# Kernel tuning notes

Hardware: AMD Instinct MI355X
Metric: run time of the kernel (lower is better)

## Reference

```python
import jax, jax.numpy as jnp
import numpy as np

B = 65536
NC = 64          # coarse samples
NF = 128         # fine samples
NEAR, FAR = 2.0, 6.0


def setup_inputs() -> dict:
    key = jax.random.key(0)
    k1, k2, k3, k4, k5, k6 = jax.random.split(key, 6)
    ray_origin = jax.random.normal(k1, (B, 3), dtype=jnp.float32)
    ray_direction = jax.random.normal(k2, (B, 3), dtype=jnp.float32)
    # stratified linspace depths, as in the coarse branch of _sample_points_on_ray
    step = (FAR - NEAR) / (NC - 1)
    coarse_depth_values = jnp.broadcast_to(
        NEAR + jnp.arange(NC, dtype=jnp.float32) * step, (B, NC)
    )
    coarse_weights = jax.random.uniform(k3, (B, NC), dtype=jnp.float32)
    u = jax.random.uniform(k4, (B, NF), dtype=jnp.float32)
    raw_density = jax.random.uniform(k5, (B, NC + NF, 1), dtype=jnp.float32)
    raw_color = jax.random.uniform(k6, (B, NC + NF, 3), dtype=jnp.float32)
    return {
        "ray_origin": ray_origin,
        "ray_direction": ray_direction,
        "coarse_depth_values": coarse_depth_values,
        "coarse_weights": coarse_weights,
        "u": u,
        "raw_density": raw_density,
        "raw_color": raw_color,
    }


def _sample_pdf(bins, weights, u):
    """Inverse-CDF sampling. bins: [B, M+1], weights: [B, M], u: [B, N]."""
    M = weights.shape[1]
    weights = weights + 1e-5
    pdf = weights / jnp.sum(weights, axis=-1, keepdims=True)
    cdf = jnp.cumsum(pdf, axis=-1)                     # [B, M]
    cdf = jnp.concatenate([jnp.zeros_like(cdf[:, :1]), cdf], axis=-1)  # [B, M+1]
    # torch loop `above_inds += (u >= cdf[:, i])` for i in [0, M) ==
    # searchsorted(cdf[:, :M], u, side='right')
    above = jax.vmap(lambda c, uu: jnp.searchsorted(c, uu, side="right"))(
        cdf[:, :M], u
    )                                                  # [B, N], values in [1, M]
    below = jnp.clip(above - 1, 0, None)
    cdf_b = jnp.take_along_axis(cdf, below, axis=-1)
    cdf_a = jnp.take_along_axis(cdf, above, axis=-1)
    bins_b = jnp.take_along_axis(bins, below, axis=-1)
    bins_a = jnp.take_along_axis(bins, above, axis=-1)
    denom = cdf_a - cdf_b
    denom = jnp.where(denom < 1e-5, jnp.ones_like(denom), denom)
    t = (u - cdf_b) / denom
    return bins_b + t * (bins_a - bins_b)


def _composite(raw_density, raw_color, depth_values):
    # distances between consecutive samples, last one = 1e10
    dists = depth_values[..., 1:] - depth_values[..., :-1]
    dists = jnp.concatenate(
        [dists, jnp.full_like(dists[:, :1], 1e10)], axis=-1
    )
    alpha = 1.0 - jnp.exp(-raw_density[..., 0] * dists)          # [B, S]
    T = jnp.cumprod(1.0 - alpha + 1e-10, axis=-1)[:, :-1]
    T = jnp.concatenate([jnp.ones_like(T[:, :1]), T], axis=-1)
    weights = T * alpha                                           # [B, S]
    depth = jnp.sum(weights * depth_values, axis=-1, keepdims=True)
    color = jnp.sum(weights[..., None] * raw_color, axis=-2)      # [B, 3]
    return depth, color, weights


def reference(ray_origin, ray_direction, coarse_depth_values, coarse_weights,
              u, raw_density, raw_color):
    # fine branch of _sample_points_on_ray
    mids = 0.5 * (coarse_depth_values[..., 1:] + coarse_depth_values[..., :-1])
    w = coarse_weights[:, 1:-1]
    fine_depths = _sample_pdf(mids, w, u)                         # [B, NF]
    depth_values = jnp.sort(
        jnp.concatenate([coarse_depth_values, fine_depths], axis=-1), axis=-1
    )                                                             # [B, NC+NF]
    points_on_ray = (
        ray_origin[:, None, :]
        + ray_direction[:, None, :] * depth_values[..., None]
    )                                                             # [B, S, 3]
    depth, color_map, weights = _composite(raw_density, raw_color, depth_values)
    # forward of RenderRay returns the color map; points kept live via dummy use
    del points_on_ray, depth, weights
    return color_map
```

## Files before the change

### kernel.cpp

```cpp
#include <hip/hip_runtime.h>

#define NC 64
#define NF 128
#define NT 192
#define B_TOTAL 65536
#define RPB 4

#define NEAR_F 2.0f
#define STEP_F (4.0f / 63.0f)
#define INV_STEP (63.0f / 4.0f)

__global__ __launch_bounds__(256) void render_ray_kernel(
    const float* __restrict__ cw,
    const float* __restrict__ u_in,
    const float* __restrict__ dens,
    const float* __restrict__ col,
    float* __restrict__ out)
{
    const int wave = threadIdx.x >> 6;
    const int lane = threadIdx.x & 63;
    const int ray  = blockIdx.x * RPB + wave;

    __shared__ float s_cdf [RPB][64];
    __shared__ float s_m   [RPB][200];
    __shared__ int   s_hist[RPB][64];

    const float wraw = cw[(size_t)ray * NC + lane];
    float x = u_in[(size_t)ray * NF + lane];
    float y = u_in[(size_t)ray * NF + 64 + lane];

    const float wv = (lane >= 1 && lane <= 62) ? (wraw + 1e-5f) : 0.0f;
    float ssum = wv;
    #pragma unroll
    for (int off = 32; off; off >>= 1) ssum += __shfl_xor(ssum, off);
    const float pdf = __fdividef(wv, ssum);
    float scan = pdf;
    #pragma unroll
    for (int off = 1; off < 64; off <<= 1) {
        const float t = __shfl_up(scan, off);
        if (lane >= off) scan += t;
    }
    s_cdf[wave][lane]  = scan;
    s_hist[wave][lane] = 0;
    __syncthreads();

    #pragma unroll
    for (int k = 2; k <= 128; k <<= 1) {
        #pragma unroll
        for (int j = k >> 1; j > 0; j >>= 1) {
            if (j == 64) {
                const float mn = fminf(x, y);
                const float mx = fmaxf(x, y);
                x = mn; y = mx;
            } else {
                const bool lower = (lane & j) == 0;
                const bool ascx  = (k >= 128) ? true : ((lane & k) == 0);
                const bool ascy  = (k >= 128) ? true
                                 : ((k == 64) ? false : ((lane & k) == 0));
                const float px = __shfl_xor(x, j);
                const float py = __shfl_xor(y, j);
                x = (ascx == lower) ? fminf(x, px) : fmaxf(x, px);
                y = (ascy == lower) ? fminf(y, py) : fmaxf(y, py);
            }
        }
    }

    const float* __restrict__ cdfp = s_cdf[wave];
    auto sample = [&](float u) -> float {
        int l = 0, h = 62;
        while (l < h) {
            const int mid = (l + h) >> 1;
            if (cdfp[mid] <= u) l = mid + 1; else h = mid;
        }
        const int below = l - 1;
        const float cb = cdfp[below];
        const float ca = cdfp[l];
        float denom = ca - cb;
        if (denom < 1e-5f) denom = 1.0f;
        const float t = __fdividef(u - cb, denom);
        return NEAR_F + ((float)below + 0.5f + t) * STEP_F;
    };

    const float fx = sample(x);
    const float fy = sample(y);
    int gx = (int)floorf((fx - NEAR_F) * INV_STEP) + 1;
    int gy = (int)floorf((fy - NEAR_F) * INV_STEP) + 1;
    gx = min(max(gx, 1), 63);
    gy = min(max(gy, 1), 63);

    s_m[wave][lane + gx]      = fx;
    s_m[wave][lane + 64 + gy] = fy;
    atomicAdd(&s_hist[wave][gx], 1);
    atomicAdd(&s_hist[wave][gy], 1);
    __syncthreads();

    int hsum = s_hist[wave][lane];
    #pragma unroll
    for (int off = 1; off < 64; off <<= 1) {
        const int t = __shfl_up(hsum, off);
        if (lane >= off) hsum += t;
    }
    s_m[wave][lane + hsum] = NEAR_F + (float)lane * STEP_F;
    __syncthreads();

    const float* __restrict__ mp = s_m[wave];
    const int i0 = 3 * lane;
    const float m0 = mp[i0], m1 = mp[i0 + 1], m2 = mp[i0 + 2];
    const float m3 = mp[i0 + 3];
    const float d0 = m1 - m0;
    const float d1 = m2 - m1;
    const float d2 = (lane == 63) ? 1e10f : (m3 - m2);

    const float* __restrict__ dp = dens + (size_t)ray * NT + i0;
    const float a0 = 1.0f - __expf(-dp[0] * d0);
    const float a1 = 1.0f - __expf(-dp[1] * d1);
    const float a2 = 1.0f - __expf(-dp[2] * d2);
    const float f0 = 1.0f - a0 + 1e-10f;
    const float f1 = 1.0f - a1 + 1e-10f;
    const float f2 = 1.0f - a2 + 1e-10f;

    float scanp = f0 * f1 * f2;
    #pragma unroll
    for (int off = 1; off < 64; off <<= 1) {
        const float t = __shfl_up(scanp, off);
        if (lane >= off) scanp *= t;
    }
    float T0 = __shfl_up(scanp, 1);
    if (lane == 0) T0 = 1.0f;
    const float T1 = T0 * f0;
    const float T2 = T1 * f1;

    const float w0 = T0 * (1.0f - f0 + 1e-10f);
    const float w1 = T1 * (1.0f - f1 + 1e-10f);
    const float w2 = T2 * (1.0f - f2 + 1e-10f);

    const float* __restrict__ cp = col + (size_t)ray * NT * 3 + 3 * (size_t)i0;
    float ax = w0 * cp[0] + w1 * cp[3] + w2 * cp[6];
    float ay = w0 * cp[1] + w1 * cp[4] + w2 * cp[7];
    float az = w0 * cp[2] + w1 * cp[5] + w2 * cp[8];

    #pragma unroll
    for (int off = 32; off; off >>= 1) {
        ax += __shfl_xor(ax, off);
        ay += __shfl_xor(ay, off);
        az += __shfl_xor(az, off);
    }
    if (lane == 0) {
        out[(size_t)ray * 3 + 0] = ax;
        out[(size_t)ray * 3 + 1] = ay;
        out[(size_t)ray * 3 + 2] = az;
    }
}

extern "C" void kernel_launch(void* const* d_in, const int* in_sizes, int n_in,
                              void* d_out, int out_size, void* d_ws, size_t ws_size,
                              hipStream_t stream) {
    const float* cwts = (const float*)d_in[3];
    const float* u    = (const float*)d_in[4];
    const float* dens = (const float*)d_in[5];
    const float* col  = (const float*)d_in[6];
    float* out = (float*)d_out;

    dim3 grid(B_TOTAL / RPB);
    dim3 block(256);
    hipLaunchKernelGGL(render_ray_kernel, grid, block, 0, stream,
                       cwts, u, dens, col, out);
}
```

Baseline: 285.9 us.

## Use DPP wave scans, wave-level barriers, and branchless fixed-depth search

Replaces the shuffle-based prefix scans with DPP row_shr/row_bcast scans and swaps the block-wide __syncthreads for wave barriers, since each wave works on its own ray and shared slice. It also makes the binary search a fixed-depth unrolled loop, computes the insertion bin directly from the interpolation fraction instead of a floor of the depth, and simplifies the bitonic compare-select logic. This cuts ds_bpermute traffic and block synchronisation stalls, but relies on wave64 DPP semantics and on the rewritten bin computation agreeing with the old one at bin boundaries.

After: 291.3 us. Within noise of the previous version (+1.9%).

```diff
diff --git a/kernel.cpp b/kernel.cpp
--- a/kernel.cpp
+++ b/kernel.cpp
@@ -8,7 +8,49 @@
 
 #define NEAR_F 2.0f
 #define STEP_F (4.0f / 63.0f)
-#define INV_STEP (63.0f / 4.0f)
+
+template<int CTRL, int RM>
+__device__ __forceinline__ float updpp_f(float oldv, float v) {
+    return __int_as_float(__builtin_amdgcn_update_dpp(
+        __float_as_int(oldv), __float_as_int(v), CTRL, RM, 0xf, false));
+}
+template<int CTRL, int RM>
+__device__ __forceinline__ int updpp_i(int oldv, int v) {
+    return __builtin_amdgcn_update_dpp(oldv, v, CTRL, RM, 0xf, false);
+}
+
+__device__ __forceinline__ float wave_iscan_add_f(float v) {
+    v += updpp_f<0x111, 0xf>(0.0f, v);
+    v += updpp_f<0x112, 0xf>(0.0f, v);
+    v += updpp_f<0x114, 0xf>(0.0f, v);
+    v += updpp_f<0x118, 0xf>(0.0f, v);
+    v += updpp_f<0x142, 0xa>(0.0f, v);
+    v += updpp_f<0x143, 0xc>(0.0f, v);
+    return v;
+}
+__device__ __forceinline__ float wave_iscan_mul_f(float v) {
+    v *= updpp_f<0x111, 0xf>(1.0f, v);
+    v *= updpp_f<0x112, 0xf>(1.0f, v);
+    v *= updpp_f<0x114, 0xf>(1.0f, v);
+    v *= updpp_f<0x118, 0xf>(1.0f, v);
+    v *= updpp_f<0x142, 0xa>(1.0f, v);
+    v *= updpp_f<0x143, 0xc>(1.0f, v);
+    return v;
+}
+__device__ __forceinline__ int wave_iscan_add_i(int v) {
+    v += updpp_i<0x111, 0xf>(0, v);
+    v += updpp_i<0x112, 0xf>(0, v);
+    v += updpp_i<0x114, 0xf>(0, v);
+    v += updpp_i<0x118, 0xf>(0, v);
+    v += updpp_i<0x142, 0xa>(0, v);
+    v += updpp_i<0x143, 0xc>(0, v);
+    return v;
+}
+
+__device__ __forceinline__ void wave_fence() {
+    __builtin_amdgcn_wave_barrier();
+    __asm__ volatile("" ::: "memory");
+}
 
 __global__ __launch_bounds__(256) void render_ray_kernel(
     const float* __restrict__ cw,
@@ -34,15 +76,9 @@
     #pragma unroll
     for (int off = 32; off; off >>= 1) ssum += __shfl_xor(ssum, off);
     const float pdf = __fdividef(wv, ssum);
-    float scan = pdf;
-    #pragma unroll
-    for (int off = 1; off < 64; off <<= 1) {
-        const float t = __shfl_up(scan, off);
-        if (lane >= off) scan += t;
-    }
-    s_cdf[wave][lane]  = scan;
+    s_cdf[wave][lane]  = wave_iscan_add_f(pdf);
     s_hist[wave][lane] = 0;
-    __syncthreads();
+    wave_fence();
 
     #pragma unroll
     for (int k = 2; k <= 128; k <<= 1) {
@@ -53,55 +89,51 @@
                 const float mx = fmaxf(x, y);
                 x = mn; y = mx;
             } else {
-                const bool lower = (lane & j) == 0;
-                const bool ascx  = (k >= 128) ? true : ((lane & k) == 0);
-                const bool ascy  = (k >= 128) ? true
-                                 : ((k == 64) ? false : ((lane & k) == 0));
+                const bool up = (lane & j) != 0;
+                const bool dx = (lane & k) != 0;
+                const bool dy = ((lane + 64) & k) != 0;
                 const float px = __shfl_xor(x, j);
                 const float py = __shfl_xor(y, j);
-                x = (ascx == lower) ? fminf(x, px) : fmaxf(x, px);
-                y = (ascy == lower) ? fminf(y, py) : fmaxf(y, py);
+                const bool cx = x < px;
+                const bool cy = y < py;
+                x = ((cx != up) != dx) ? x : px;
+                y = ((cy != up) != dy) ? y : py;
             }
         }
     }
 
     const float* __restrict__ cdfp = s_cdf[wave];
-    auto sample = [&](float u) -> float {
-        int l = 0, h = 62;
-        while (l < h) {
-            const int mid = (l + h) >> 1;
-            if (cdfp[mid] <= u) l = mid + 1; else h = mid;
+    auto sample = [&](float u, int& g) -> float {
+        int l = 0;
+        #pragma unroll
+        for (int s = 32; s; s >>= 1) {
+            const int t = l + s;
+            if (cdfp[t - 1] <= u) l = t;
         }
+        l = min(l, 62);
         const int below = l - 1;
         const float cb = cdfp[below];
         const float ca = cdfp[l];
         float denom = ca - cb;
         if (denom < 1e-5f) denom = 1.0f;
         const float t = __fdividef(u - cb, denom);
+        g = below + 1 + ((t >= 0.5f) ? 1 : 0);
         return NEAR_F + ((float)below + 0.5f + t) * STEP_F;
     };
 
-    const float fx = sample(x);
-    const float fy = sample(y);
-    int gx = (int)floorf((fx - NEAR_F) * INV_STEP) + 1;
-    int gy = (int)floorf((fy - NEAR_F) * INV_STEP) + 1;
-    gx = min(max(gx, 1), 63);
-    gy = min(max(gy, 1), 63);
+    int gx, gy;
+    const float fx = sample(x, gx);
+    const float fy = sample(y, gy);
 
     s_m[wave][lane + gx]      = fx;
     s_m[wave][lane + 64 + gy] = fy;
     atomicAdd(&s_hist[wave][gx], 1);
     atomicAdd(&s_hist[wave][gy], 1);
-    __syncthreads();
+    wave_fence();
 
-    int hsum = s_hist[wave][lane];
-    #pragma unroll
-    for (int off = 1; off < 64; off <<= 1) {
-        const int t = __shfl_up(hsum, off);
-        if (lane >= off) hsum += t;
-    }
+    const int hsum = wave_iscan_add_i(s_hist[wave][lane]);
     s_m[wave][lane + hsum] = NEAR_F + (float)lane * STEP_F;
-    __syncthreads();
+    wave_fence();
 
     const float* __restrict__ mp = s_m[wave];
     const int i0 = 3 * lane;
@@ -119,12 +151,7 @@
     const float f1 = 1.0f - a1 + 1e-10f;
     const float f2 = 1.0f - a2 + 1e-10f;
 
-    float scanp = f0 * f1 * f2;
-    #pragma unroll
-    for (int off = 1; off < 64; off <<= 1) {
-        const float t = __shfl_up(scanp, off);
-        if (lane >= off) scanp *= t;
-    }
+    float scanp = wave_iscan_mul_f(f0 * f1 * f2);
     float T0 = __shfl_up(scanp, 1);
     if (lane == 0) T0 = 1.0f;
     const float T1 = T0 * f0;
```
